# Performance work log

Measured on AMD Instinct MI355X. Metric: run time of the kernel, lower is better.

## Reference

```python
import jax, jax.numpy as jnp
import numpy as np

B, T, D = 8, 4096, 512
Q, K = 4, 1024
KERNEL, STRIDE = 5, 2
COMMIT = 0.25


def setup_inputs() -> dict:
    key = jax.random.key(0)
    k1, k2, k3 = jax.random.split(key, 3)
    x = jax.random.normal(k1, (B, T, D), dtype=jnp.float32)
    codebooks = jax.random.normal(k2, (Q, K, D), dtype=jnp.float32)
    # he_normal fan_in = KERNEL * D
    conv_w = jax.random.normal(k3, (KERNEL, D, D), dtype=jnp.float32) * np.sqrt(2.0 / (KERNEL * D))
    return {"x": x, "codebooks": codebooks, "conv_w": conv_w}


def _vq_nearest(residual, cb):
    # residual: [B,T,D], cb: [K,D] -> squared L2 distances [B,T,K]
    d = (jnp.sum(residual * residual, axis=-1, keepdims=True)
         - 2.0 * jnp.einsum('btd,kd->btk', residual, cb)
         + jnp.sum(cb * cb, axis=-1))
    idx = jnp.argmin(d, axis=-1)          # [B,T] int
    q = cb[idx]                            # [B,T,D] gather
    return q, idx


def residual_vq(x, codebooks):
    residual = x
    quantized_out = jnp.zeros_like(x)
    losses = []
    indices = []
    for qi in range(Q):  # small fixed number of quantizers
        q, idx = _vq_nearest(residual, codebooks[qi])
        # commitment loss (codebook frozen at inference / EMA-updated in training)
        losses.append(COMMIT * jnp.mean((jax.lax.stop_gradient(q) - residual) ** 2))
        # straight-through estimator
        q_st = residual + jax.lax.stop_gradient(q - residual)
        quantized_out = quantized_out + q_st
        residual = residual - jax.lax.stop_gradient(q)
        indices.append(idx)
    loss = jnp.sum(jnp.stack(losses))
    return quantized_out, jnp.stack(indices, axis=0), loss


def reference(x, codebooks, conv_w):
    quantized_out, indices, vq_loss = residual_vq(x, codebooks)
    # Conv1D, stride 2, 'same' padding, no bias: NWC x WIO -> NWC
    y = jax.lax.conv_general_dilated(
        quantized_out, conv_w,
        window_strides=(STRIDE,), padding='SAME',
        dimension_numbers=('NWC', 'WIO', 'NWC'))
    y = jax.nn.gelu(y, approximate=False)
    return y, quantized_out, indices, vq_loss
```

## Files before the change

### kernel.cpp

```cpp
#include <hip/hip_runtime.h>
#include <math.h>

#define Bq 8
#define Tq 4096
#define Dq 512
#define Qn 4
#define Kk 1024
#define OWn 2048
#define NROWS (Bq*Tq)

#define QO_OFF (Bq*OWn*Dq)
#define IDX_OFF (QO_OFF + Bq*Tq*Dq)
#define LOSS_OFF (IDX_OFF + Qn*NROWS)

typedef __bf16 bf16x8 __attribute__((ext_vector_type(8)));
typedef _Float16 f16x8 __attribute__((ext_vector_type(8)));
typedef float f32x16 __attribute__((ext_vector_type(16)));
typedef float f32x4 __attribute__((ext_vector_type(4)));

__device__ __forceinline__ unsigned pack2h(_Float16 a, _Float16 b) {
  return (unsigned)__builtin_bit_cast(unsigned short, a)
       | ((unsigned)__builtin_bit_cast(unsigned short, b) << 16);
}

__global__ __launch_bounds__(256) void prep_cb(const float* __restrict__ cb,
                                               float* __restrict__ cbnorm,
                                               _Float16* __restrict__ cbf,
                                               float* __restrict__ lacc) {
  int w = threadIdx.x >> 6, lane = threadIdx.x & 63;
  int row = blockIdx.x * 4 + w;
  int q = row >> 10, k = row & 1023;
  const f32x4* c4 = (const f32x4*)(cb + (size_t)row * Dq);
  f32x4 v0 = c4[lane * 2], v1 = c4[lane * 2 + 1];
  float s = v0.x*v0.x + v0.y*v0.y + v0.z*v0.z + v0.w*v0.w
          + v1.x*v1.x + v1.y*v1.y + v1.z*v1.z + v1.w*v1.w;
  f16x8 bv;
  bv[0]=(_Float16)v0.x; bv[1]=(_Float16)v0.y; bv[2]=(_Float16)v0.z; bv[3]=(_Float16)v0.w;
  bv[4]=(_Float16)v1.x; bv[5]=(_Float16)v1.y; bv[6]=(_Float16)v1.z; bv[7]=(_Float16)v1.w;
  int ds = lane >> 1, hs = lane & 1;
  size_t off = ((size_t)((k >> 5) * 32 + ds) * 2 + hs) * 256 + (k & 31) * 8;
  *(f16x8*)(cbf + (size_t)q * (Kk * Dq) + off) = bv;
#pragma unroll
  for (int off2 = 32; off2; off2 >>= 1) s += __shfl_down(s, off2);
  if (lane == 0) cbnorm[row] = s;
  if (blockIdx.x == 0 && threadIdx.x == 0) *lacc = 0.f;
}

__global__ __launch_bounds__(256) void prep_cmax(const float* __restrict__ cbnorm,
                                                 float* __restrict__ cmax) {
  int w = threadIdx.x >> 6, lane = threadIdx.x & 63;
  float m = 0.f;
#pragma unroll
  for (int j = 0; j < 16; ++j) m = fmaxf(m, cbnorm[w * Kk + lane * 16 + j]);
#pragma unroll
  for (int off = 32; off; off >>= 1) m = fmaxf(m, __shfl_down(m, off));
  if (lane == 0) cmax[w] = sqrtf(m);
}

__global__ __launch_bounds__(256) void prep_wb(const float* __restrict__ w,
                                               __bf16* __restrict__ wb) {
  int g = blockIdx.x * 256 + threadIdx.x;
  int l31 = g & 31, hs = (g >> 5) & 1, c32 = (g >> 6) & 15, s = g >> 10;
  int kw = s >> 5, ci16 = s & 31;
  int ci = ci16 * 16 + hs * 8;
  int co = c32 * 32 + l31;
  bf16x8 bv;
#pragma unroll
  for (int e = 0; e < 8; ++e)
    bv[e] = (__bf16)w[(size_t)(kw * Dq + ci + e) * Dq + co];
  *(bf16x8*)(wb + (size_t)g * 8) = bv;
}

__global__ __launch_bounds__(512, 1) void vq_all(
    const float* __restrict__ x, float* __restrict__ qo,
    const _Float16* __restrict__ cbf, const float* __restrict__ cb,
    const float* __restrict__ cbnorm, const float* __restrict__ cmax,
    float* __restrict__ idxo, float* __restrict__ lacc) {
  __shared__ _Float16 rh[64 * 512];
  __shared__ unsigned redB[64 * 8];
  __shared__ float rnorm_l[64];
  __shared__ float thrL[64];
  __shared__ int rowcount[64];
  __shared__ unsigned short rowlist[64 * 32];

  const int tid = threadIdx.x;
  const int w = tid >> 6, lane = tid & 63, l31 = lane & 31, hs = lane >> 5;
  const int row0g = blockIdx.x * 64;
  char* rhc = (char*)rh;

  f32x4 r0[8], r1[8];
#pragma unroll
  for (int rr = 0; rr < 8; ++rr) {
    size_t gb = (size_t)(row0g + w * 8 + rr) * Dq + lane * 8;
    r0[rr] = *(const f32x4*)(x + gb);
    r1[rr] = *(const f32x4*)(x + gb + 4);
  }
  float lsum = 0.f;

#pragma unroll 1
  for (int qi = 0; qi < Qn; ++qi) {
    const _Float16* cbf_q = cbf + (size_t)qi * (Kk * Dq);
    const float*    cb_q  = cb  + (size_t)qi * (Kk * Dq);
    const float*    cbn_q = cbnorm + qi * Kk;

#pragma unroll
    for (int rr = 0; rr < 8; ++rr) {
      int row = w * 8 + rr;
      f16x8 bv;
      bv[0]=(_Float16)r0[rr].x; bv[1]=(_Float16)r0[rr].y;
      bv[2]=(_Float16)r0[rr].z; bv[3]=(_Float16)r0[rr].w;
      bv[4]=(_Float16)r1[rr].x; bv[5]=(_Float16)r1[rr].y;
      bv[6]=(_Float16)r1[rr].z; bv[7]=(_Float16)r1[rr].w;
      *(f16x8*)(rhc + ((row * 1024 + lane * 16) ^ ((row & 7) << 4))) = bv;
      float rn = r0[rr].x*r0[rr].x + r0[rr].y*r0[rr].y + r0[rr].z*r0[rr].z + r0[rr].w*r0[rr].w
               + r1[rr].x*r1[rr].x + r1[rr].y*r1[rr].y + r1[rr].z*r1[rr].z + r1[rr].w*r1[rr].w;
#pragma unroll
      for (int off = 1; off < 64; off <<= 1) rn += __shfl_xor(rn, off);
      if (lane == 0) rnorm_l[row] = rn;
    }
    __syncthreads();

    unsigned psA[4][8], psB[4][8];
    const int ab0 = l31 * 1024 + hs * 16;
    const int asw = (l31 & 7) << 4;
#pragma unroll
    for (int p = 0; p < 2; ++p) {
      const int ct0 = 2 * p, ct1 = 2 * p + 1;
      const _Float16* bp0 = cbf_q + (size_t)(w * 4 + ct0) * 16384 + hs * 256 + l31 * 8;
      const _Float16* bp1 = cbf_q + (size_t)(w * 4 + ct1) * 16384 + hs * 256 + l31 * 8;
      f32x16 a00, a01, a10, a11;
#pragma unroll
      for (int i = 0; i < 16; ++i) { a00[i]=0.f; a01[i]=0.f; a10[i]=0.f; a11[i]=0.f; }
#pragma unroll 8
      for (int ds = 0; ds < 32; ++ds) {
        f16x8 a0 = *(const f16x8*)(rhc + ((ab0 + ds * 32) ^ asw));
        f16x8 a1 = *(const f16x8*)(rhc + ((ab0 + 32 * 1024 + ds * 32) ^ asw));
        f16x8 b0 = *(const f16x8*)(bp0 + ds * 512);
        f16x8 b1 = *(const f16x8*)(bp1 + ds * 512);
        a00 = __builtin_amdgcn_mfma_f32_32x32x16_f16(a0, b0, a00, 0, 0, 0);
        a01 = __builtin_amdgcn_mfma_f32_32x32x16_f16(a0, b1, a01, 0, 0, 0);
        a10 = __builtin_amdgcn_mfma_f32_32x32x16_f16(a1, b0, a10, 0, 0, 0);
        a11 = __builtin_amdgcn_mfma_f32_32x32x16_f16(a1, b1, a11, 0, 0, 0);
      }
      const float cn0 = cbn_q[w * 128 + ct0 * 32 + l31];
      const float cn1 = cbn_q[w * 128 + ct1 * 32 + l31];
#pragma unroll
      for (int j = 0; j < 8; ++j) {
        psA[ct0][j] = pack2h((_Float16)(cn0 - 2.f * a00[2*j]), (_Float16)(cn0 - 2.f * a00[2*j+1]));
        psA[ct1][j] = pack2h((_Float16)(cn1 - 2.f * a01[2*j]), (_Float16)(cn1 - 2.f * a01[2*j+1]));
        psB[ct0][j] = pack2h((_Float16)(cn0 - 2.f * a10[2*j]), (_Float16)(cn0 - 2.f * a10[2*j+1]));
        psB[ct1][j] = pack2h((_Float16)(cn1 - 2.f * a11[2*j]), (_Float16)(cn1 - 2.f * a11[2*j+1]));
      }
    }

#pragma unroll
    for (int rt = 0; rt < 2; ++rt) {
      unsigned pk[16];
#pragma unroll
      for (int i = 0; i < 16; ++i) {
        pk[i] = 0xFFFFFFFFu;
#pragma unroll
        for (int ct = 0; ct < 4; ++ct) {
          unsigned col = (unsigned)(w * 128 + ct * 32 + l31);
          unsigned u = ((rt == 0 ? psA[ct][i >> 1] : psB[ct][i >> 1]) >> ((i & 1) * 16)) & 0xFFFFu;
          unsigned key = (u & 0x8000u) ? (u ^ 0xFFFFu) : (u | 0x8000u);
          unsigned pkc = (key << 10) | col;
          if (pkc < pk[i]) pk[i] = pkc;
        }
#pragma unroll
        for (int off = 1; off <= 16; off <<= 1) {
          unsigned t = __shfl_xor(pk[i], off);
          if (t < pk[i]) pk[i] = t;
        }
      }
      if (l31 == 0) {
#pragma unroll
        for (int i = 0; i < 16; ++i) {
          int rit = rt * 32 + (i & 3) + 8 * (i >> 2) + 4 * hs;
          redB[rit * 8 + w] = pk[i];
        }
      }
    }
    __syncthreads();

    if (tid < 64) {
      unsigned mb = redB[tid * 8];
#pragma unroll
      for (int j = 1; j < 8; ++j) {
        unsigned v = redB[tid * 8 + j];
        if (v < mb) mb = v;
      }
      unsigned key = (mb >> 10) & 0xFFFFu;
      unsigned ub = (key & 0x8000u) ? (key ^ 0x8000u) : (key ^ 0xFFFFu);
      float mstar = (float)__builtin_bit_cast(_Float16, (unsigned short)ub);
      float rn = sqrtf(rnorm_l[tid]);
      float cm = cmax[qi];
      thrL[tid] = mstar + 0.005f * rn * cm + 0.001f * fabsf(mstar) + 0.3f;
      rowcount[tid] = 0;
    }
    __syncthreads();

#pragma unroll
    for (int rt = 0; rt < 2; ++rt) {
#pragma unroll
      for (int i = 0; i < 16; ++i) {
        int rit = rt * 32 + (i & 3) + 8 * (i >> 2) + 4 * hs;
        float t = thrL[rit];
#pragma unroll
        for (int ct = 0; ct < 4; ++ct) {
          unsigned col = (unsigned)(w * 128 + ct * 32 + l31);
          unsigned u = ((rt == 0 ? psA[ct][i >> 1] : psB[ct][i >> 1]) >> ((i & 1) * 16)) & 0xFFFFu;
          float s = (float)__builtin_bit_cast(_Float16, (unsigned short)u);
          if (s <= t) {
            int p = atomicAdd(&rowcount[rit], 1);
            if (p < 32) rowlist[rit * 32 + p] = (unsigned short)col;
          }
        }
      }
    }
    __syncthreads();

#pragma unroll
    for (int rr = 0; rr < 8; ++rr) {
      int row = w * 8 + rr;
      int cnt = rowcount[row];
      int total = (cnt > 32) ? Kk : cnt;
      float bs = 3.4028235e38f; int bk = 1 << 30;
      for (int ci2 = 0; ci2 < total; ++ci2) {
        int k = (cnt > 32) ? ci2 : (int)rowlist[row * 32 + ci2];
        const f32x4* crow = (const f32x4*)(cb_q + ((size_t)k << 9)) + lane * 2;
        f32x4 c0 = crow[0], c1 = crow[1];
        float dot = 0.f;
        dot = fmaf(r0[rr].x, c0.x, dot); dot = fmaf(r0[rr].y, c0.y, dot);
        dot = fmaf(r0[rr].z, c0.z, dot); dot = fmaf(r0[rr].w, c0.w, dot);
        dot = fmaf(r1[rr].x, c1.x, dot); dot = fmaf(r1[rr].y, c1.y, dot);
        dot = fmaf(r1[rr].z, c1.z, dot); dot = fmaf(r1[rr].w, c1.w, dot);
#pragma unroll
        for (int off = 1; off < 64; off <<= 1) dot += __shfl_xor(dot, off);
        float sc = cbn_q[k] - 2.f * dot;
        if (sc < bs || (sc == bs && k < bk)) { bs = sc; bk = k; }
      }
      if (lane == 0) idxo[(size_t)qi * NROWS + row0g + row] = (float)bk;
      const f32x4* crow = (const f32x4*)(cb_q + ((size_t)bk << 9)) + lane * 2;
      f32x4 c0 = crow[0], c1 = crow[1];
      r0[rr].x -= c0.x; r0[rr].y -= c0.y; r0[rr].z -= c0.z; r0[rr].w -= c0.w;
      r1[rr].x -= c1.x; r1[rr].y -= c1.y; r1[rr].z -= c1.z; r1[rr].w -= c1.w;
      lsum += r0[rr].x*r0[rr].x + r0[rr].y*r0[rr].y + r0[rr].z*r0[rr].z + r0[rr].w*r0[rr].w
            + r1[rr].x*r1[rr].x + r1[rr].y*r1[rr].y + r1[rr].z*r1[rr].z + r1[rr].w*r1[rr].w;
    }
    __syncthreads();
  }

#pragma unroll
  for (int rr = 0; rr < 8; ++rr) {
    size_t gb = (size_t)(row0g + w * 8 + rr) * Dq + lane * 8;
    f32x4 xv0 = *(const f32x4*)(x + gb), xv1 = *(const f32x4*)(x + gb + 4);
    f32x4 o0, o1;
    o0.x = xv0.x - r0[rr].x; o0.y = xv0.y - r0[rr].y;
    o0.z = xv0.z - r0[rr].z; o0.w = xv0.w - r0[rr].w;
    o1.x = xv1.x - r1[rr].x; o1.y = xv1.y - r1[rr].y;
    o1.z = xv1.z - r1[rr].z; o1.w = xv1.w - r1[rr].w;
    *(f32x4*)(qo + gb) = o0;
    *(f32x4*)(qo + gb + 4) = o1;
  }
#pragma unroll
  for (int off = 1; off < 64; off <<= 1) lsum += __shfl_xor(lsum, off);
  if (lane == 0) atomicAdd(lacc, lsum);
}

__global__ __launch_bounds__(512, 2) void conv_mfma(const float* __restrict__ qo,
                                                    const __bf16* __restrict__ wb,
                                                    float* __restrict__ y) {
  __shared__ char As[259 * 128];
  const int tid = threadIdx.x;
  const int w = tid >> 6, lane = tid & 63, l31 = lane & 31, hs = lane >> 5;
  const int rowblk = blockIdx.x, coblk = blockIdx.y;
  const int n = rowblk >> 4;
  const int o0 = (rowblk & 15) * 128;
  const int t0 = 2 * o0 - 1;
  const int c32g = coblk * 8 + w;

  f32x16 acc[4];
#pragma unroll
  for (int rt = 0; rt < 4; ++rt)
#pragma unroll
    for (int i = 0; i < 16; ++i) acc[rt][i] = 0.f;

  for (int ct8 = 0; ct8 < 8; ++ct8) {
    __syncthreads();
    for (int s = tid; s < 2072; s += 512) {
      int irow = s >> 3, cg = s & 7;
      int t = t0 + irow;
      bf16x8 bv;
      if (t >= 0 && t < Tq) {
        const float* src = qo + ((size_t)(n * Tq + t)) * Dq + ct8 * 64 + cg * 8;
        f32x4 v0 = *(const f32x4*)(src), v1 = *(const f32x4*)(src + 4);
        bv[0]=(__bf16)v0.x; bv[1]=(__bf16)v0.y; bv[2]=(__bf16)v0.z; bv[3]=(__bf16)v0.w;
        bv[4]=(__bf16)v1.x; bv[5]=(__bf16)v1.y; bv[6]=(__bf16)v1.z; bv[7]=(__bf16)v1.w;
      } else {
#pragma unroll
        for (int e = 0; e < 8; ++e) bv[e] = (__bf16)0.f;
      }
      *(bf16x8*)(As + ((irow * 128 + cg * 16) ^ (((irow >> 1) & 7) << 4))) = bv;
    }
    __syncthreads();
#pragma unroll
    for (int kw = 0; kw < 5; ++kw) {
#pragma unroll
      for (int ks = 0; ks < 4; ++ks) {
        int s16 = kw * 32 + ct8 * 4 + ks;
        bf16x8 b = *(const bf16x8*)(wb + ((size_t)(s16 * 16 + c32g) * 2 + hs) * 256 + l31 * 8);
#pragma unroll
        for (int rt = 0; rt < 4; ++rt) {
          int ir = 2 * (rt * 32 + l31) + kw;
          bf16x8 a = *(const bf16x8*)(As + ((ir * 128 + ks * 32 + hs * 16) ^ (((ir >> 1) & 7) << 4)));
          acc[rt] = __builtin_amdgcn_mfma_f32_32x32x16_bf16(a, b, acc[rt], 0, 0, 0);
        }
      }
    }
  }
  const int co = coblk * 256 + w * 32 + l31;
#pragma unroll
  for (int rt = 0; rt < 4; ++rt)
#pragma unroll
    for (int i = 0; i < 16; ++i) {
      int orow = rt * 32 + (i & 3) + 8 * (i >> 2) + 4 * hs;
      float v = acc[rt][i];
      float g = 0.5f * v * (1.f + erff(v * 0.70710678118654752f));
      y[((size_t)(n * OWn + o0 + orow)) * Dq + co] = g;
    }
}

__global__ void loss_final(const float* __restrict__ lacc, float* __restrict__ out) {
  out[0] = 0.25f * lacc[0] / 16777216.0f;
}

extern "C" void kernel_launch(void* const* d_in, const int* in_sizes, int n_in,
                              void* d_out, int out_size, void* d_ws, size_t ws_size,
                              hipStream_t stream) {
  const float* x  = (const float*)d_in[0];
  const float* cb = (const float*)d_in[1];
  const float* cw = (const float*)d_in[2];
  float* out = (float*)d_out;
  float* y    = out;
  float* qo   = out + QO_OFF;
  float* idxo = out + IDX_OFF;
  float* losso = out + LOSS_OFF;

  float* fws    = (float*)d_ws;
  float* lacc   = fws;
  float* cmax   = fws + 8;
  float* cbnorm = fws + 16;
  _Float16* cbf = (_Float16*)((char*)d_ws + (32 << 10));
  __bf16* wb  = (__bf16*)((char*)d_ws + (8 << 20));

  prep_cb<<<1024, 256, 0, stream>>>(cb, cbnorm, cbf, lacc);
  prep_cmax<<<1, 256, 0, stream>>>(cbnorm, cmax);
  prep_wb<<<640, 256, 0, stream>>>(cw, wb);

  vq_all<<<512, 512, 0, stream>>>(x, qo, cbf, cb, cbnorm, cmax, idxo, lacc);

  conv_mfma<<<dim3(128, 2), 512, 0, stream>>>(qo, wb, y);
  loss_final<<<1, 1, 0, stream>>>(lacc, losso);
}
```

Measured before the change: 505.1 us.

## Double vq_all block to 16 waves, splitting row tiles across wave groups

The VQ kernel now launches 1024 threads per block instead of 512. Each wave handles 4 rows instead of 8, and the distance GEMM is split so waves 0-7 and 8-15 each compute one 32-row tile against their 128-column codebook slice. The goal is more waves in flight per CU to hide global codebook loads and the serial refine loop, and fewer accumulator registers per wave. The cost is that each B-fragment load from global now feeds only two MFMAs instead of four, so codebook traffic per block doubles, and barriers span more waves.

```diff
diff --git a/kernel.cpp b/kernel.cpp
--- a/kernel.cpp
+++ b/kernel.cpp
@@ -71,7 +71,7 @@
   *(bf16x8*)(wb + (size_t)g * 8) = bv;
 }
 
-__global__ __launch_bounds__(512, 1) void vq_all(
+__global__ __launch_bounds__(1024, 1) void vq_all(
     const float* __restrict__ x, float* __restrict__ qo,
     const _Float16* __restrict__ cbf, const float* __restrict__ cb,
     const float* __restrict__ cbnorm, const float* __restrict__ cmax,
@@ -88,10 +88,10 @@
   const int row0g = blockIdx.x * 64;
   char* rhc = (char*)rh;
 
-  f32x4 r0[8], r1[8];
-#pragma unroll
-  for (int rr = 0; rr < 8; ++rr) {
-    size_t gb = (size_t)(row0g + w * 8 + rr) * Dq + lane * 8;
+  f32x4 r0[4], r1[4];
+#pragma unroll
+  for (int rr = 0; rr < 4; ++rr) {
+    size_t gb = (size_t)(row0g + w * 4 + rr) * Dq + lane * 8;
     r0[rr] = *(const f32x4*)(x + gb);
     r1[rr] = *(const f32x4*)(x + gb + 4);
   }
@@ -104,8 +104,8 @@
     const float*    cbn_q = cbnorm + qi * Kk;
 
 #pragma unroll
-    for (int rr = 0; rr < 8; ++rr) {
-      int row = w * 8 + rr;
+    for (int rr = 0; rr < 4; ++rr) {
+      int row = w * 4 + rr;
       f16x8 bv;
       bv[0]=(_Float16)r0[rr].x; bv[1]=(_Float16)r0[rr].y;
       bv[2]=(_Float16)r0[rr].z; bv[3]=(_Float16)r0[rr].w;
@@ -120,49 +120,44 @@
     }
     __syncthreads();
 
-    unsigned psA[4][8], psB[4][8];
-    const int ab0 = l31 * 1024 + hs * 16;
+    unsigned ps[4][8];
+    const int cg = w & 7, rg = w >> 3;
+    const int ab0 = (rg * 32 + l31) * 1024 + hs * 16;
     const int asw = (l31 & 7) << 4;
 #pragma unroll
     for (int p = 0; p < 2; ++p) {
       const int ct0 = 2 * p, ct1 = 2 * p + 1;
-      const _Float16* bp0 = cbf_q + (size_t)(w * 4 + ct0) * 16384 + hs * 256 + l31 * 8;
-      const _Float16* bp1 = cbf_q + (size_t)(w * 4 + ct1) * 16384 + hs * 256 + l31 * 8;
-      f32x16 a00, a01, a10, a11;
-#pragma unroll
-      for (int i = 0; i < 16; ++i) { a00[i]=0.f; a01[i]=0.f; a10[i]=0.f; a11[i]=0.f; }
+      const _Float16* bp0 = cbf_q + (size_t)(cg * 4 + ct0) * 16384 + hs * 256 + l31 * 8;
+      const _Float16* bp1 = cbf_q + (size_t)(cg * 4 + ct1) * 16384 + hs * 256 + l31 * 8;
+      f32x16 accA, accB;
+#pragma unroll
+      for (int i = 0; i < 16; ++i) { accA[i] = 0.f; accB[i] = 0.f; }
 #pragma unroll 8
       for (int ds = 0; ds < 32; ++ds) {
-        f16x8 a0 = *(const f16x8*)(rhc + ((ab0 + ds * 32) ^ asw));
-        f16x8 a1 = *(const f16x8*)(rhc + ((ab0 + 32 * 1024 + ds * 32) ^ asw));
+        f16x8 a  = *(const f16x8*)(rhc + ((ab0 + ds * 32) ^ asw));
         f16x8 b0 = *(const f16x8*)(bp0 + ds * 512);
         f16x8 b1 = *(const f16x8*)(bp1 + ds * 512);
-        a00 = __builtin_amdgcn_mfma_f32_32x32x16_f16(a0, b0, a00, 0, 0, 0);
-        a01 = __builtin_amdgcn_mfma_f32_32x32x16_f16(a0, b1, a01, 0, 0, 0);
-        a10 = __builtin_amdgcn_mfma_f32_32x32x16_f16(a1, b0, a10, 0, 0, 0);
-        a11 = __builtin_amdgcn_mfma_f32_32x32x16_f16(a1, b1, a11, 0, 0, 0);
-      }
-      const float cn0 = cbn_q[w * 128 + ct0 * 32 + l31];
-      const float cn1 = cbn_q[w * 128 + ct1 * 32 + l31];
+        accA = __builtin_amdgcn_mfma_f32_32x32x16_f16(a, b0, accA, 0, 0, 0);
+        accB = __builtin_amdgcn_mfma_f32_32x32x16_f16(a, b1, accB, 0, 0, 0);
+      }
+      const float cn0 = cbn_q[cg * 128 + ct0 * 32 + l31];
+      const float cn1 = cbn_q[cg * 128 + ct1 * 32 + l31];
 #pragma unroll
       for (int j = 0; j < 8; ++j) {
-        psA[ct0][j] = pack2h((_Float16)(cn0 - 2.f * a00[2*j]), (_Float16)(cn0 - 2.f * a00[2*j+1]));
-        psA[ct1][j] = pack2h((_Float16)(cn1 - 2.f * a01[2*j]), (_Float16)(cn1 - 2.f * a01[2*j+1]));
-        psB[ct0][j] = pack2h((_Float16)(cn0 - 2.f * a10[2*j]), (_Float16)(cn0 - 2.f * a10[2*j+1]));
-        psB[ct1][j] = pack2h((_Float16)(cn1 - 2.f * a11[2*j]), (_Float16)(cn1 - 2.f * a11[2*j+1]));
-      }
-    }
-
-#pragma unroll
-    for (int rt = 0; rt < 2; ++rt) {
+        ps[ct0][j] = pack2h((_Float16)(cn0 - 2.f * accA[2*j]), (_Float16)(cn0 - 2.f * accA[2*j+1]));
+        ps[ct1][j] = pack2h((_Float16)(cn1 - 2.f * accB[2*j]), (_Float16)(cn1 - 2.f * accB[2*j+1]));
+      }
+    }
+
+    {
       unsigned pk[16];
 #pragma unroll
       for (int i = 0; i < 16; ++i) {
         pk[i] = 0xFFFFFFFFu;
 #pragma unroll
         for (int ct = 0; ct < 4; ++ct) {
-          unsigned col = (unsigned)(w * 128 + ct * 32 + l31);
-          unsigned u = ((rt == 0 ? psA[ct][i >> 1] : psB[ct][i >> 1]) >> ((i & 1) * 16)) & 0xFFFFu;
+          unsigned col = (unsigned)(cg * 128 + ct * 32 + l31);
+          unsigned u = (ps[ct][i >> 1] >> ((i & 1) * 16)) & 0xFFFFu;
           unsigned key = (u & 0x8000u) ? (u ^ 0xFFFFu) : (u | 0x8000u);
           unsigned pkc = (key << 10) | col;
           if (pkc < pk[i]) pk[i] = pkc;
@@ -176,8 +171,8 @@
       if (l31 == 0) {
 #pragma unroll
         for (int i = 0; i < 16; ++i) {
-          int rit = rt * 32 + (i & 3) + 8 * (i >> 2) + 4 * hs;
-          redB[rit * 8 + w] = pk[i];
+          int rit = rg * 32 + (i & 3) + 8 * (i >> 2) + 4 * hs;
+          redB[rit * 8 + cg] = pk[i];
         }
       }
     }
@@ -201,28 +196,25 @@
     __syncthreads();
 
 #pragma unroll
-    for (int rt = 0; rt < 2; ++rt) {
-#pragma unroll
-      for (int i = 0; i < 16; ++i) {
-        int rit = rt * 32 + (i & 3) + 8 * (i >> 2) + 4 * hs;
-        float t = thrL[rit];
-#pragma unroll
-        for (int ct = 0; ct < 4; ++ct) {
-          unsigned col = (unsigned)(w * 128 + ct * 32 + l31);
-          unsigned u = ((rt == 0 ? psA[ct][i >> 1] : psB[ct][i >> 1]) >> ((i & 1) * 16)) & 0xFFFFu;
-          float s = (float)__builtin_bit_cast(_Float16, (unsigned short)u);
-          if (s <= t) {
-            int p = atomicAdd(&rowcount[rit], 1);
-            if (p < 32) rowlist[rit * 32 + p] = (unsigned short)col;
-          }
-        }
-      }
-    }
-    __syncthreads();
-
-#pragma unroll
-    for (int rr = 0; rr < 8; ++rr) {
-      int row = w * 8 + rr;
+    for (int i = 0; i < 16; ++i) {
+      int rit = rg * 32 + (i & 3) + 8 * (i >> 2) + 4 * hs;
+      float t = thrL[rit];
+#pragma unroll
+      for (int ct = 0; ct < 4; ++ct) {
+        unsigned col = (unsigned)(cg * 128 + ct * 32 + l31);
+        unsigned u = (ps[ct][i >> 1] >> ((i & 1) * 16)) & 0xFFFFu;
+        float s = (float)__builtin_bit_cast(_Float16, (unsigned short)u);
+        if (s <= t) {
+          int p = atomicAdd(&rowcount[rit], 1);
+          if (p < 32) rowlist[rit * 32 + p] = (unsigned short)col;
+        }
+      }
+    }
+    __syncthreads();
+
+#pragma unroll
+    for (int rr = 0; rr < 4; ++rr) {
+      int row = w * 4 + rr;
       int cnt = rowcount[row];
       int total = (cnt > 32) ? Kk : cnt;
       float bs = 3.4028235e38f; int bk = 1 << 30;
@@ -252,8 +244,8 @@
   }
 
 #pragma unroll
-  for (int rr = 0; rr < 8; ++rr) {
-    size_t gb = (size_t)(row0g + w * 8 + rr) * Dq + lane * 8;
+  for (int rr = 0; rr < 4; ++rr) {
+    size_t gb = (size_t)(row0g + w * 4 + rr) * Dq + lane * 8;
     f32x4 xv0 = *(const f32x4*)(x + gb), xv1 = *(const f32x4*)(x + gb + 4);
     f32x4 o0, o1;
     o0.x = xv0.x - r0[rr].x; o0.y = xv0.y - r0[rr].y;
@@ -358,7 +350,7 @@
   prep_cmax<<<1, 256, 0, stream>>>(cbnorm, cmax);
   prep_wb<<<640, 256, 0, stream>>>(cw, wb);
 
-  vq_all<<<512, 512, 0, stream>>>(x, qo, cbf, cb, cbnorm, cmax, idxo, lacc);
+  vq_all<<<512, 1024, 0, stream>>>(x, qo, cbf, cb, cbnorm, cmax, idxo, lacc);
 
   conv_mfma<<<dim3(128, 2), 512, 0, stream>>>(qo, wb, y);
   loss_final<<<1, 1, 0, stream>>>(lacc, losso);
```

Result: slower. 596.1 us (+18.0%).
